# Kernel optimization log

Hardware: AMD Instinct MI355X
Metric: run time of the kernel (lower is better)

## Reference

```python
import jax, jax.numpy as jnp
import numpy as np

N = 100000      # nodes
E = 1600000     # edges
H = 4           # num_heads
D = 16          # hidden_size per head
F_IN = 128      # input_size
HD = H * D
EPS = 1e-5


def setup_inputs() -> dict:
    key = jax.random.key(0)
    ks = jax.random.split(key, 12)
    s = 1.0 / np.sqrt(F_IN)
    feature = jax.random.normal(ks[0], (N, F_IN), jnp.float32)
    src = jax.random.randint(ks[1], (E,), 0, N, jnp.int32)
    dst = jax.random.randint(ks[2], (E,), 0, N, jnp.int32)
    Wq = jax.random.normal(ks[3], (F_IN, HD), jnp.float32) * s
    bq = jnp.zeros((HD,), jnp.float32)
    Wk = jax.random.normal(ks[4], (F_IN, HD), jnp.float32) * s
    bk = jnp.zeros((HD,), jnp.float32)
    Wv = jax.random.normal(ks[5], (F_IN, HD), jnp.float32) * s
    bv = jnp.zeros((HD,), jnp.float32)
    Wskip = jax.random.normal(ks[6], (F_IN, HD), jnp.float32) * s
    bskip = jnp.zeros((HD,), jnp.float32)
    ln_g = jnp.ones((HD,), jnp.float32)
    ln_b = jnp.zeros((HD,), jnp.float32)
    return dict(feature=feature, src=src, dst=dst, Wq=Wq, bq=bq, Wk=Wk, bk=bk,
                Wv=Wv, bv=bv, Wskip=Wskip, bskip=bskip, ln_g=ln_g, ln_b=ln_b)


def reference(feature, src, dst, Wq, bq, Wk, bk, Wv, bv, Wskip, bskip, ln_g, ln_b):
    # QKV projections, [N, H, D]; q scaled by 1/sqrt(D) (as in send_recv)
    q = ((feature @ Wq) + bq).reshape(N, H, D) * (1.0 / np.sqrt(D))
    k = ((feature @ Wk) + bk).reshape(N, H, D)
    v = ((feature @ Wv) + bv).reshape(N, H, D)
    # edge scores: sum over head dim of q[dst] * k[src] -> [E, H]
    alpha = jnp.sum(q[dst] * k[src], axis=-1)
    # segment softmax over incoming edges of each destination node
    m = jax.ops.segment_max(alpha, dst, num_segments=N)          # [N, H]
    ex = jnp.exp(alpha - m[dst])                                 # [E, H]
    z = jax.ops.segment_sum(ex, dst, num_segments=N)             # [N, H]
    a = ex / z[dst]                                              # [E, H]
    # weighted values, concat heads, scatter-sum to destination nodes
    msg = (v[src] * a[:, :, None]).reshape(E, HD)                # [E, H*D]
    out = jax.ops.segment_sum(msg, dst, num_segments=N)          # [N, H*D]
    # skip connection (no gate)
    out = out + (feature @ Wskip) + bskip
    # layer norm over last dim
    mu = jnp.mean(out, axis=-1, keepdims=True)
    var = jnp.mean(jnp.square(out - mu), axis=-1, keepdims=True)
    out = (out - mu) * jax.lax.rsqrt(var + EPS) * ln_g + ln_b
    return out
```

## Files before the change

### kernel.cpp

```cpp
#include <hip/hip_runtime.h>

typedef unsigned short u16;
typedef __attribute__((ext_vector_type(8))) short short8;
typedef __attribute__((ext_vector_type(4))) float f32x4;

#define N_NODES 100000
#define N_EDGES 1600000
#define F_IN    128
#define HD      64
#define LN_EPS  1e-5f

#define SCAN_BLOCKS  98
#define PROJ_TOTAL   1563
#define PROJ_A       625
#define PH1_GRID     6875
#define PH2_GRID     7813

__device__ u16 g_WT[4 * HD * F_IN];

__device__ __forceinline__ float bf2f(u16 u) {
    union { unsigned int i; float f; } x;
    x.i = ((unsigned int)u) << 16;
    return x.f;
}
__device__ __forceinline__ u16 f2bf(float f) {
    unsigned int u;
    __builtin_memcpy(&u, &f, 4);
    unsigned int r = u + 0x7FFFu + ((u >> 16) & 1u);
    return (u16)(r >> 16);
}
__device__ __forceinline__ void ld4m(const void* p, int idx, float o[4]) {
    const float4 v = *reinterpret_cast<const float4*>((const float*)p + idx);
    o[0] = v.x; o[1] = v.y; o[2] = v.z; o[3] = v.w;
}

__device__ __forceinline__ void proj_body(
    int pid, int mode,
    const void* feature,
    const void* Wq, const void* bq, const void* Wk, const void* bk,
    const void* Wv, const void* bv, const void* Ws, const void* bs,
    u16* Qb, unsigned int* KV, u16* Sb,
    u16* lq, u16* lk, u16* lv, u16* ls)
{
    const int tid  = threadIdx.x;
    const int w    = tid >> 6;
    const int lane = tid & 63;

    const void* W;
    const void* b;
    float scale = 1.0f;
    if      (w == 0) { W = Wq; b = bq; scale = 0.25f; }
    else if (w == 1) { W = Wk; b = bk; }
    else if (w == 2) { W = Wv; b = bv; }
    else             { W = Ws; b = bs; }

    if (mode == 0) {
        const u16* F = (const u16*)feature;
        const int h = lane >> 4;
        const int c = lane & 15;

        const u16* WT = g_WT + w * HD * F_IN;
        short8 wfrag[4][4];
        #pragma unroll
        for (int ct = 0; ct < 4; ++ct) {
            const int col = ct * 16 + c;
            #pragma unroll
            for (int ks = 0; ks < 4; ++ks)
                wfrag[ct][ks] = *reinterpret_cast<const short8*>(
                    WT + col * F_IN + ks * 32 + h * 8);
        }

        float bias_f[4][4];
        #pragma unroll
        for (int ct = 0; ct < 4; ++ct) {
            const ushort4 bu =
                *reinterpret_cast<const ushort4*>((const u16*)b + ct * 16 + h * 4);
            bias_f[ct][0] = bf2f(bu.x); bias_f[ct][1] = bf2f(bu.y);
            bias_f[ct][2] = bf2f(bu.z); bias_f[ct][3] = bf2f(bu.w);
        }

        u16* Lmine = (w == 0) ? lq : (w == 1) ? lk : (w == 2) ? lv : ls;

        short8 fr[2][4];
        {
            const size_t arow = (size_t)(pid * 64 + c) * F_IN;
            #pragma unroll
            for (int ks = 0; ks < 4; ++ks)
                fr[0][ks] = *reinterpret_cast<const short8*>(F + arow + ks * 32 + h * 8);
        }

        #pragma unroll
        for (int t = 0; t < 4; ++t) {
            const int nbase = pid * 64 + t * 16;
            if (nbase >= N_NODES) break;
            const int cur = t & 1, nxt = cur ^ 1;

            const int nb2 = nbase + 16;
            if (t < 3 && nb2 < N_NODES) {
                const size_t arow = (size_t)(nb2 + c) * F_IN;
                #pragma unroll
                for (int ks = 0; ks < 4; ++ks)
                    fr[nxt][ks] =
                        *reinterpret_cast<const short8*>(F + arow + ks * 32 + h * 8);
            }

            f32x4 acc[4];
            #pragma unroll
            for (int ct = 0; ct < 4; ++ct) acc[ct] = (f32x4){0.f, 0.f, 0.f, 0.f};
            #pragma unroll
            for (int ks = 0; ks < 4; ++ks)
                #pragma unroll
                for (int ct = 0; ct < 4; ++ct)
                    acc[ct] = __builtin_amdgcn_mfma_f32_16x16x32_bf16(
                        wfrag[ct][ks], fr[cur][ks], acc[ct], 0, 0, 0);

            #pragma unroll
            for (int ct = 0; ct < 4; ++ct) {
                ushort4 pk;
                pk.x = f2bf((acc[ct][0] + bias_f[ct][0]) * scale);
                pk.y = f2bf((acc[ct][1] + bias_f[ct][1]) * scale);
                pk.z = f2bf((acc[ct][2] + bias_f[ct][2]) * scale);
                pk.w = f2bf((acc[ct][3] + bias_f[ct][3]) * scale);
                const int bo = (ct * 32 + h * 8) ^ ((c & 7) << 4);
                *reinterpret_cast<ushort4*>(
                    reinterpret_cast<char*>(Lmine) + c * 128 + bo) = pk;
            }
            __syncthreads();

            {
                const int half = tid >> 7;
                const int tt   = tid & 127;
                const int row  = tt >> 3, seg = tt & 7;
                const int ro   = (seg * 16) ^ ((row & 7) << 4);
                const uint4 qs = *reinterpret_cast<const uint4*>(
                    reinterpret_cast<const char*>(half ? ls : lq) + row * 128 + ro);
                *reinterpret_cast<uint4*>(
                    (half ? Sb : Qb) + (size_t)(nbase + row) * HD + seg * 8) = qs;

                const int krow = tid >> 4, c4 = tid & 15;
                const int ko   = (c4 * 8) ^ ((krow & 7) << 4);
                const ushort4 kk = *reinterpret_cast<const ushort4*>(
                    reinterpret_cast<const char*>(lk) + krow * 128 + ko);
                const ushort4 vv = *reinterpret_cast<const ushort4*>(
                    reinterpret_cast<const char*>(lv) + krow * 128 + ko);
                uint4 o;
                o.x = (unsigned)kk.x | ((unsigned)vv.x << 16);
                o.y = (unsigned)kk.y | ((unsigned)vv.y << 16);
                o.z = (unsigned)kk.z | ((unsigned)vv.z << 16);
                o.w = (unsigned)kk.w | ((unsigned)vv.w << 16);
                *reinterpret_cast<uint4*>(
                    KV + (size_t)(nbase + krow) * HD + c4 * 4) = o;
            }
            __syncthreads();
        }
    } else {
        const int colg  = lane & 15;
        const int nodeg = lane >> 4;
        const int c0    = colg * 4;
        const int kvsub = (w == 1) ? 0 : 1;
        u16* KVu = (u16*)KV;

        for (int st = 0; st < 4; ++st) {
            if (pid * 64 + st * 16 >= N_NODES) break;
            const int node_base = pid * 64 + st * 16 + nodeg * 4;

            float acc[4][4];
            #pragma unroll
            for (int n = 0; n < 4; ++n)
                #pragma unroll
                for (int cc = 0; cc < 4; ++cc) acc[n][cc] = 0.f;

            for (int k = 0; k < F_IN; k += 4) {
                float wv4[4][4];
                #pragma unroll
                for (int kk = 0; kk < 4; ++kk)
                    ld4m(W, (k + kk) * HD + c0, wv4[kk]);
                #pragma unroll
                for (int n = 0; n < 4; ++n) {
                    float f[4];
                    ld4m(feature, (node_base + n) * F_IN + k, f);
                    #pragma unroll
                    for (int cc = 0; cc < 4; ++cc)
                        acc[n][cc] += f[0] * wv4[0][cc] + f[1] * wv4[1][cc]
                                    + f[2] * wv4[2][cc] + f[3] * wv4[3][cc];
                }
            }

            float bias[4];
            ld4m(b, c0, bias);

            #pragma unroll
            for (int n = 0; n < 4; ++n) {
                const int node = node_base + n;
                u16 r[4];
                #pragma unroll
                for (int cc = 0; cc < 4; ++cc)
                    r[cc] = f2bf((acc[n][cc] + bias[cc]) * scale);

                if (w == 0 || w == 3) {
                    u16* O = (w == 0) ? Qb : Sb;
                    ushort4 u4; u4.x = r[0]; u4.y = r[1]; u4.z = r[2]; u4.w = r[3];
                    *reinterpret_cast<ushort4*>(O + (size_t)node * HD + c0) = u4;
                } else {
                    #pragma unroll
                    for (int cc = 0; cc < 4; ++cc)
                        KVu[(size_t)node * 2 * HD + 2 * (c0 + cc) + kvsub] = r[cc];
                }
            }
        }
    }
}

__global__ __launch_bounds__(256) void tiny0_r15(
    const void* __restrict__ Wq, const void* __restrict__ Wk,
    const void* __restrict__ Wv, const void* __restrict__ Ws,
    const u16* __restrict__ feat, int* __restrict__ mode)
{
    const int bid = blockIdx.x;
    if (bid < 16) {
        const int m  = bid >> 2;
        const int kg = bid & 3;
        const u16* W = (const u16*)((m == 0) ? Wq : (m == 1) ? Wk
                                  : (m == 2) ? Wv : Ws);
        const int t  = threadIdx.x;
        const int k  = kg * 32 + (t >> 3);
        const int c0 = (t & 7) * 8;
        union { uint4 v; u16 s[8]; } row;
        row.v = *reinterpret_cast<const uint4*>(W + k * HD + c0);
        u16* outp = g_WT + m * HD * F_IN;
        #pragma unroll
        for (int j = 0; j < 8; ++j)
            outp[(c0 + j) * F_IN + k] = row.s[j];
    } else {
        const int lane = threadIdx.x;
        if (lane < 64) {
            float mx = 0.f;
            #pragma unroll
            for (int i = 0; i < 4; ++i)
                mx = fmaxf(mx, fabsf(bf2f(feat[lane * 4 + i])));
            #pragma unroll
            for (int o = 1; o < 64; o <<= 1) mx = fmaxf(mx, __shfl_xor(mx, o));
            if (lane == 0) *mode = (mx > 1000.f) ? 1 : 0;
        }
    }
}

__global__ __launch_bounds__(256) void ph1_r15(
    const void* __restrict__ feature,
    const void* __restrict__ Wq, const void* __restrict__ bq,
    const void* __restrict__ Wk, const void* __restrict__ bk,
    const void* __restrict__ Wv, const void* __restrict__ bv,
    const void* __restrict__ Ws, const void* __restrict__ bs,
    u16* __restrict__ Qb, unsigned int* __restrict__ KV, u16* __restrict__ Sb,
    const int* __restrict__ mode_p,
    const int* __restrict__ dst, int* __restrict__ deg)
{
    __shared__ u16 lq[16 * 64];
    __shared__ u16 lk[16 * 64];
    __shared__ u16 lv[16 * 64];
    __shared__ u16 ls[16 * 64];

    const int bid = blockIdx.x;
    if (bid % 11 != 0) {
        const int hid = bid - bid / 11 - 1;
        const int e = hid * 256 + threadIdx.x;
        if (e < N_EDGES) atomicAdd(&deg[dst[e]], 1);
        return;
    }
    proj_body(bid / 11, *mode_p, feature, Wq, bq, Wk, bk, Wv, bv, Ws, bs,
              Qb, KV, Sb, lq, lk, lv, ls);
}

__global__ __launch_bounds__(1024) void scanA_r15(const int* __restrict__ deg,
                                                  int* __restrict__ off,
                                                  int* __restrict__ bsum)
{
    __shared__ int wsum[16];
    __shared__ int wexcl[16];
    const int tid = threadIdx.x, lane = tid & 63, wid = tid >> 6;
    const int idx = blockIdx.x * 1024 + tid;
    const int v = (idx < N_NODES) ? deg[idx] : 0;
    int sc = v;
    #pragma unroll
    for (int o = 1; o < 64; o <<= 1) {
        int t = __shfl_up(sc, o);
        if (lane >= o) sc += t;
    }
    if (lane == 63) wsum[wid] = sc;
    __syncthreads();
    if (tid == 0) {
        int run = 0;
        for (int i = 0; i < 16; ++i) { wexcl[i] = run; run += wsum[i]; }
        bsum[blockIdx.x] = run;
    }
    __syncthreads();
    if (idx < N_NODES) off[idx] = wexcl[wid] + (sc - v);
}

__global__ __launch_bounds__(1024) void scanC_r15(const int* __restrict__ deg,
                                                  int* __restrict__ off,
                                                  int* __restrict__ woff,
                                                  const int* __restrict__ bsum)
{
    __shared__ int base_s;
    const int tid = threadIdx.x;
    const int bid = blockIdx.x;
    if (tid == 0) {
        int run = 0;
        for (int i = 0; i < bid; ++i) run += bsum[i];
        base_s = run;
    }
    __syncthreads();
    const int base = base_s;
    const int idx = bid * 1024 + tid;
    if (idx < N_NODES) {
        const int e = off[idx] + base;
        off[idx]  = e;
        woff[idx] = e;
        if (idx == N_NODES - 1) off[N_NODES] = e + deg[idx];
    }
}

__global__ __launch_bounds__(256) void ph2_r15(
    const void* __restrict__ feature,
    const void* __restrict__ Wq, const void* __restrict__ bq,
    const void* __restrict__ Wk, const void* __restrict__ bk,
    const void* __restrict__ Wv, const void* __restrict__ bv,
    const void* __restrict__ Ws, const void* __restrict__ bs,
    u16* __restrict__ Qb, unsigned int* __restrict__ KV, u16* __restrict__ Sb,
    const int* __restrict__ mode_p,
    const int* __restrict__ src, const int* __restrict__ dst,
    int* __restrict__ woff, int* __restrict__ srcs)
{
    __shared__ u16 lq[16 * 64];
    __shared__ u16 lk[16 * 64];
    __shared__ u16 lv[16 * 64];
    __shared__ u16 ls[16 * 64];

    const int bid = blockIdx.x;
    if (bid % 5 != 0) {
        const int sid = bid - bid / 5 - 1;
        const int e = sid * 256 + threadIdx.x;
        if (e < N_EDGES) {
            const int d = dst[e];
            const int pos = atomicAdd(&woff[d], 1);
            srcs[pos] = src[e];
        }
        return;
    }
    const int pid = PROJ_A + bid / 5;
    if (pid >= PROJ_TOTAL) return;
    proj_body(pid, *mode_p, feature, Wq, bq, Wk, bk, Wv, bv, Ws, bs,
              Qb, KV, Sb, lq, lk, lv, ls);
}

__global__ __launch_bounds__(256) void attn_r15(
    const u16* __restrict__ Qb, const unsigned int* __restrict__ KV,
    const u16* __restrict__ Sb,
    const int* __restrict__ off, const int* __restrict__ srcs,
    const void* __restrict__ ln_g, const void* __restrict__ ln_b,
    void* __restrict__ out, const int* __restrict__ mode_p)
{
    const int mode = *mode_p;
    const int node = blockIdx.x * 4 + (threadIdx.x >> 6);
    const int lane = threadIdx.x & 63;

    const float qv = bf2f(Qb[(size_t)node * HD + lane]);
    const int e0 = off[node], e1 = off[node + 1];

    float z = 0.f, acc = 0.f;
    for (int base = e0; base < e1; base += 64) {
        const int n_e = min(64, e1 - base);
        int sidx = (base + lane < e1) ? srcs[base + lane] : 0;
        sidx = (sidx < 0) ? 0 : ((sidx >= N_NODES) ? N_NODES - 1 : sidx);
        int i = 0;
        for (; i + 8 <= n_e; i += 8) {
            unsigned int kv[8];
            float p[8];
            #pragma unroll
            for (int j = 0; j < 8; ++j) {
                const int s = __shfl(sidx, i + j);
                kv[j] = KV[(size_t)s * HD + lane];
            }
            #pragma unroll
            for (int j = 0; j < 8; ++j)
                p[j] = qv * bf2f((u16)(kv[j] & 0xffffu));
            #pragma unroll
            for (int m = 1; m < 16; m <<= 1) {
                #pragma unroll
                for (int j = 0; j < 8; ++j) p[j] += __shfl_xor(p[j], m);
            }
            float zp = 0.f, ap = 0.f;
            #pragma unroll
            for (int j = 0; j < 8; ++j) {
                const float x = __expf(p[j]);
                zp += x;
                ap += x * bf2f((u16)(kv[j] >> 16));
            }
            z += zp; acc += ap;
        }
        for (; i + 4 <= n_e; i += 4) {
            unsigned int kv[4];
            float p[4];
            #pragma unroll
            for (int j = 0; j < 4; ++j) {
                const int s = __shfl(sidx, i + j);
                kv[j] = KV[(size_t)s * HD + lane];
            }
            #pragma unroll
            for (int j = 0; j < 4; ++j)
                p[j] = qv * bf2f((u16)(kv[j] & 0xffffu));
            #pragma unroll
            for (int m = 1; m < 16; m <<= 1) {
                #pragma unroll
                for (int j = 0; j < 4; ++j) p[j] += __shfl_xor(p[j], m);
            }
            #pragma unroll
            for (int j = 0; j < 4; ++j) {
                const float x = __expf(p[j]);
                z   += x;
                acc += x * bf2f((u16)(kv[j] >> 16));
            }
        }
        for (; i < n_e; ++i) {
            const int s = __shfl(sidx, i);
            const unsigned int kv = KV[(size_t)s * HD + lane];
            float p = qv * bf2f((u16)(kv & 0xffffu));
            #pragma unroll
            for (int m = 1; m < 16; m <<= 1) p += __shfl_xor(p, m);
            const float ex = __expf(p);
            z   += ex;
            acc += ex * bf2f((u16)(kv >> 16));
        }
    }

    const float msg = (e1 > e0) ? (acc / z) : 0.f;
    float t = msg + bf2f(Sb[(size_t)node * HD + lane]);

    float mu = t;
    #pragma unroll
    for (int m = 1; m < 64; m <<= 1) mu += __shfl_xor(mu, m);
    mu *= (1.f / 64.f);
    const float d = t - mu;
    float var = d * d;
    #pragma unroll
    for (int m = 1; m < 64; m <<= 1) var += __shfl_xor(var, m);
    var *= (1.f / 64.f);
    const float r = d * rsqrtf(var + LN_EPS);

    const float g  = mode ? ((const float*)ln_g)[lane] : bf2f(((const u16*)ln_g)[lane]);
    const float bb = mode ? ((const float*)ln_b)[lane] : bf2f(((const u16*)ln_b)[lane]);
    const float res = r * g + bb;
    const size_t o = (size_t)node * HD + lane;
    if (mode) ((float*)out)[o] = res;
    else      ((u16*)out)[o]   = f2bf(res);
}

extern "C" void kernel_launch(void* const* d_in, const int* in_sizes, int n_in,
                              void* d_out, int out_size, void* d_ws, size_t ws_size,
                              hipStream_t stream)
{
    const void* feature = d_in[0];
    const int*  src     = (const int*)d_in[1];
    const int*  dst     = (const int*)d_in[2];
    const void* Wq = d_in[3];  const void* bq = d_in[4];
    const void* Wk = d_in[5];  const void* bk = d_in[6];
    const void* Wv = d_in[7];  const void* bv = d_in[8];
    const void* Ws = d_in[9];  const void* bs = d_in[10];
    const void* ln_g = d_in[11];
    const void* ln_b = d_in[12];

    u16* Qb = (u16*)d_ws;
    unsigned int* KV = (unsigned int*)(Qb + (size_t)N_NODES * HD);
    u16* Sb = (u16*)(KV + (size_t)N_NODES * HD);
    int* deg  = (int*)(Sb + (size_t)N_NODES * HD);
    int* off  = deg + N_NODES;
    int* woff = off + (N_NODES + 1);
    int* srcs = woff + N_NODES;
    int* mode = srcs + N_EDGES;
    int* bsum = mode + 1;

    const size_t need = (size_t)((char*)(bsum + SCAN_BLOCKS) - (char*)d_ws);
    if (ws_size < need) return;

    hipMemsetAsync(deg, 0, N_NODES * sizeof(int), stream);

    tiny0_r15<<<dim3(17), dim3(256), 0, stream>>>(
        Wq, Wk, Wv, Ws, (const u16*)feature, mode);

    ph1_r15<<<dim3(PH1_GRID), dim3(256), 0, stream>>>(
        feature, Wq, bq, Wk, bk, Wv, bv, Ws, bs,
        Qb, KV, Sb, mode, dst, deg);

    scanA_r15<<<dim3(SCAN_BLOCKS), dim3(1024), 0, stream>>>(deg, off, bsum);
    scanC_r15<<<dim3(SCAN_BLOCKS), dim3(1024), 0, stream>>>(deg, off, woff, bsum);

    ph2_r15<<<dim3(PH2_GRID), dim3(256), 0, stream>>>(
        feature, Wq, bq, Wk, bk, Wv, bv, Ws, bs,
        Qb, KV, Sb, mode, src, dst, woff, srcs);

    attn_r15<<<dim3(N_NODES / 4), dim3(256), 0, stream>>>(
        Qb, KV, Sb, off, srcs, ln_g, ln_b, d_out, mode);
}
```

Before: 555.2 us.

## Pre-bucket edges by destination range to localize CSR scatter atomics

The degree-count pass now also appends each edge, packed as (dst low bits, src), into per-bucket sub-buffers keyed by dst/1024, with an overflow list for full buckets. The CSR fill pass then has one block per bucket drain its pairs, so the woff atomics and srcs writes for a block fall within a small node and edge range. This replaces the random global scatter over 1.6M edges with more local traffic. In exchange it adds an extra write and read of the packed pair buffer, leaves only 98 blocks doing the scatter, and adds a serial loop over sub-buckets plus an overflow scan in every bucket block.

Measured after the change: 1.017 ms. 83.1% more time.

```diff
diff --git a/kernel.cpp b/kernel.cpp
--- a/kernel.cpp
+++ b/kernel.cpp
@@ -14,7 +14,12 @@
 #define PROJ_TOTAL   1563
 #define PROJ_A       625
 #define PH1_GRID     6875
-#define PH2_GRID     7813
+#define NBUCK        98
+#define NSUB         8
+#define BCAP         3072
+#define OVF_CAP      65536
+#define PH2_PB       98
+#define PH2_GRID     1078
 
 __device__ u16 g_WT[4 * HD * F_IN];
 
@@ -211,7 +216,7 @@
     }
 }
 
-__global__ __launch_bounds__(256) void tiny0_r15(
+__global__ __launch_bounds__(256) void tiny0_r16(
     const void* __restrict__ Wq, const void* __restrict__ Wk,
     const void* __restrict__ Wv, const void* __restrict__ Ws,
     const u16* __restrict__ feat, int* __restrict__ mode)
@@ -245,7 +250,7 @@
     }
 }
 
-__global__ __launch_bounds__(256) void ph1_r15(
+__global__ __launch_bounds__(256) void ph1_r16(
     const void* __restrict__ feature,
     const void* __restrict__ Wq, const void* __restrict__ bq,
     const void* __restrict__ Wk, const void* __restrict__ bk,
@@ -253,7 +258,10 @@
     const void* __restrict__ Ws, const void* __restrict__ bs,
     u16* __restrict__ Qb, unsigned int* __restrict__ KV, u16* __restrict__ Sb,
     const int* __restrict__ mode_p,
-    const int* __restrict__ dst, int* __restrict__ deg)
+    const int* __restrict__ src, const int* __restrict__ dst,
+    int* __restrict__ deg, int* __restrict__ bcnt,
+    unsigned int* __restrict__ pairs,
+    int* __restrict__ ovf_cnt, uint2* __restrict__ ovf)
 {
     __shared__ u16 lq[16 * 64];
     __shared__ u16 lk[16 * 64];
@@ -262,16 +270,31 @@
 
     const int bid = blockIdx.x;
     if (bid % 11 != 0) {
-        const int hid = bid - bid / 11 - 1;
-        const int e = hid * 256 + threadIdx.x;
-        if (e < N_EDGES) atomicAdd(&deg[dst[e]], 1);
+        const int aid = bid - bid / 11 - 1;
+        const int e = aid * 256 + threadIdx.x;
+        if (e < N_EDGES) {
+            int s = src[e], d = dst[e];
+            s = (s < 0) ? 0 : ((s >= N_NODES) ? N_NODES - 1 : s);
+            d = (d < 0) ? 0 : ((d >= N_NODES) ? N_NODES - 1 : d);
+            atomicAdd(&deg[d], 1);
+            const int b   = d >> 10;
+            const int sub = bid & 7;
+            const int p = atomicAdd(&bcnt[b * NSUB + sub], 1);
+            if (p < BCAP) {
+                pairs[(b * NSUB + sub) * BCAP + p] =
+                    ((unsigned)(d & 1023) << 17) | (unsigned)s;
+            } else {
+                const int q = atomicAdd(ovf_cnt, 1);
+                if (q < OVF_CAP) ovf[q] = make_uint2((unsigned)s, (unsigned)d);
+            }
+        }
         return;
     }
     proj_body(bid / 11, *mode_p, feature, Wq, bq, Wk, bk, Wv, bv, Ws, bs,
               Qb, KV, Sb, lq, lk, lv, ls);
 }
 
-__global__ __launch_bounds__(1024) void scanA_r15(const int* __restrict__ deg,
+__global__ __launch_bounds__(1024) void scanA_r16(const int* __restrict__ deg,
                                                   int* __restrict__ off,
                                                   int* __restrict__ bsum)
 {
@@ -297,7 +320,7 @@
     if (idx < N_NODES) off[idx] = wexcl[wid] + (sc - v);
 }
 
-__global__ __launch_bounds__(1024) void scanC_r15(const int* __restrict__ deg,
+__global__ __launch_bounds__(1024) void scanC_r16(const int* __restrict__ deg,
                                                   int* __restrict__ off,
                                                   int* __restrict__ woff,
                                                   const int* __restrict__ bsum)
@@ -321,7 +344,7 @@
     }
 }
 
-__global__ __launch_bounds__(256) void ph2_r15(
+__global__ __launch_bounds__(256) void ph2_r16(
     const void* __restrict__ feature,
     const void* __restrict__ Wq, const void* __restrict__ bq,
     const void* __restrict__ Wk, const void* __restrict__ bk,
@@ -329,7 +352,8 @@
     const void* __restrict__ Ws, const void* __restrict__ bs,
     u16* __restrict__ Qb, unsigned int* __restrict__ KV, u16* __restrict__ Sb,
     const int* __restrict__ mode_p,
-    const int* __restrict__ src, const int* __restrict__ dst,
+    const int* __restrict__ bcnt, const unsigned int* __restrict__ pairs,
+    const int* __restrict__ ovf_cnt, const uint2* __restrict__ ovf,
     int* __restrict__ woff, int* __restrict__ srcs)
 {
     __shared__ u16 lq[16 * 64];
@@ -338,23 +362,40 @@
     __shared__ u16 ls[16 * 64];
 
     const int bid = blockIdx.x;
-    if (bid % 5 != 0) {
-        const int sid = bid - bid / 5 - 1;
-        const int e = sid * 256 + threadIdx.x;
-        if (e < N_EDGES) {
-            const int d = dst[e];
-            const int pos = atomicAdd(&woff[d], 1);
-            srcs[pos] = src[e];
+    if (bid % 11 == 0 && bid / 11 < NBUCK) {
+        const int b   = bid / 11;
+        const int tid = threadIdx.x;
+        const int nb  = b << 10;
+        #pragma unroll 1
+        for (int sub = 0; sub < NSUB; ++sub) {
+            const int n = min(bcnt[b * NSUB + sub], BCAP);
+            const unsigned int* P = pairs + (b * NSUB + sub) * BCAP;
+            for (int i = tid; i < n; i += 256) {
+                const unsigned int pk = P[i];
+                const int s = (int)(pk & 0x1FFFFu);
+                const int d = nb + (int)(pk >> 17);
+                const int pos = atomicAdd(&woff[d], 1);
+                srcs[pos] = s;
+            }
+        }
+        const int oc = min(*ovf_cnt, OVF_CAP);
+        for (int i = tid; i < oc; i += 256) {
+            const uint2 e = ovf[i];
+            if ((int)(e.y >> 10) == b) {
+                const int pos = atomicAdd(&woff[(int)e.y], 1);
+                srcs[pos] = (int)e.x;
+            }
         }
         return;
     }
-    const int pid = PROJ_A + bid / 5;
+    const int nslots = min((bid + 10) / 11, NBUCK);
+    const int pid = PROJ_A + (bid - nslots);
     if (pid >= PROJ_TOTAL) return;
     proj_body(pid, *mode_p, feature, Wq, bq, Wk, bk, Wv, bv, Ws, bs,
               Qb, KV, Sb, lq, lk, lv, ls);
 }
 
-__global__ __launch_bounds__(256) void attn_r15(
+__global__ __launch_bounds__(256) void attn_r16(
     const u16* __restrict__ Qb, const unsigned int* __restrict__ KV,
     const u16* __restrict__ Sb,
     const int* __restrict__ off, const int* __restrict__ srcs,
@@ -474,31 +515,36 @@
     unsigned int* KV = (unsigned int*)(Qb + (size_t)N_NODES * HD);
     u16* Sb = (u16*)(KV + (size_t)N_NODES * HD);
     int* deg  = (int*)(Sb + (size_t)N_NODES * HD);
-    int* off  = deg + N_NODES;
+    int* bcnt = deg + N_NODES;
+    int* ovf_cnt = bcnt + NBUCK * NSUB;
+    int* off  = ovf_cnt + 1;
     int* woff = off + (N_NODES + 1);
     int* srcs = woff + N_NODES;
     int* mode = srcs + N_EDGES;
     int* bsum = mode + 1;
-
-    const size_t need = (size_t)((char*)(bsum + SCAN_BLOCKS) - (char*)d_ws);
+    uint2* ovf = (uint2*)(bsum + SCAN_BLOCKS + 1);
+    unsigned int* pairs = (unsigned int*)(ovf + OVF_CAP);
+
+    const size_t need =
+        (size_t)((char*)(pairs + (size_t)NBUCK * NSUB * BCAP) - (char*)d_ws);
     if (ws_size < need) return;
 
-    hipMemsetAsync(deg, 0, N_NODES * sizeof(int), stream);
-
-    tiny0_r15<<<dim3(17), dim3(256), 0, stream>>>(
+    hipMemsetAsync(deg, 0, (N_NODES + NBUCK * NSUB + 1) * sizeof(int), stream);
+
+    tiny0_r16<<<dim3(17), dim3(256), 0, stream>>>(
         Wq, Wk, Wv, Ws, (const u16*)feature, mode);
 
-    ph1_r15<<<dim3(PH1_GRID), dim3(256), 0, stream>>>(
+    ph1_r16<<<dim3(PH1_GRID), dim3(256), 0, stream>>>(
         feature, Wq, bq, Wk, bk, Wv, bv, Ws, bs,
-        Qb, KV, Sb, mode, dst, deg);
-
-    scanA_r15<<<dim3(SCAN_BLOCKS), dim3(1024), 0, stream>>>(deg, off, bsum);
-    scanC_r15<<<dim3(SCAN_BLOCKS), dim3(1024), 0, stream>>>(deg, off, woff, bsum);
-
-    ph2_r15<<<dim3(PH2_GRID), dim3(256), 0, stream>>>(
+        Qb, KV, Sb, mode, src, dst, deg, bcnt, pairs, ovf_cnt, ovf);
+
+    scanA_r16<<<dim3(SCAN_BLOCKS), dim3(1024), 0, stream>>>(deg, off, bsum);
+    scanC_r16<<<dim3(SCAN_BLOCKS), dim3(1024), 0, stream>>>(deg, off, woff, bsum);
+
+    ph2_r16<<<dim3(PH2_GRID), dim3(256), 0, stream>>>(
         feature, Wq, bq, Wk, bk, Wv, bv, Ws, bs,
-        Qb, KV, Sb, mode, src, dst, woff, srcs);
-
-    attn_r15<<<dim3(N_NODES / 4), dim3(256), 0, stream>>>(
+        Qb, KV, Sb, mode, bcnt, pairs, ovf_cnt, ovf, woff, srcs);
+
+    attn_r16<<<dim3(N_NODES / 4), dim3(256), 0, stream>>>(
         Qb, KV, Sb, off, srcs, ln_g, ln_b, d_out, mode);
 }
```
